# Kernel tuning notes

Hardware: AMD Instinct MI355X
Metric: run time of the kernel (lower is better)

Reference implementation:

```python
import jax, jax.numpy as jnp
import numpy as np

N_EDGES = 1_250_000
N_NODES = 100_000
EDGE_DIM = 64
N_RADIAL = 16
OUT_DIM = 1


def setup_inputs() -> dict:
    key = jax.random.key(0)
    ks = jax.random.split(key, 12)
    s_e = 1.0 / np.sqrt(EDGE_DIM)
    s_r = 1.0 / np.sqrt(N_RADIAL)
    return {
        "x": jax.random.normal(ks[0], (N_EDGES, EDGE_DIM), jnp.float32),
        "rbf": jax.random.uniform(ks[1], (N_EDGES, N_RADIAL), jnp.float32),
        "idx_i": jax.random.randint(ks[2], (N_EDGES,), 0, N_NODES, jnp.int64),
        "num_nodes": N_NODES,
        # rbf_dense: Dense(n_radial, edge_dim, bias=False) -> weight (edge_dim, n_radial)
        "W_rbf": jax.random.normal(ks[3], (EDGE_DIM, N_RADIAL), jnp.float32) * s_r,
        # three hidden Dense(edge_dim, edge_dim) with bias
        "W1": jax.random.normal(ks[4], (EDGE_DIM, EDGE_DIM), jnp.float32) * s_e,
        "b1": jnp.zeros((EDGE_DIM,), jnp.float32),
        "W2": jax.random.normal(ks[5], (EDGE_DIM, EDGE_DIM), jnp.float32) * s_e,
        "b2": jnp.zeros((EDGE_DIM,), jnp.float32),
        "W3": jax.random.normal(ks[6], (EDGE_DIM, EDGE_DIM), jnp.float32) * s_e,
        "b3": jnp.zeros((EDGE_DIM,), jnp.float32),
        # final Dense(edge_dim, out_dim, bias=False) -> weight (out_dim, edge_dim)
        "W_out": jax.random.normal(ks[7], (OUT_DIM, EDGE_DIM), jnp.float32) * s_e,
    }


def swish(h):
    # Swish(beta=1.0): h * sigmoid(h)
    return h * jax.nn.sigmoid(h)


def reference(x, rbf, idx_i, num_nodes, W_rbf, W1, b1, W2, b2, W3, b3, W_out):
    # edge gating: Dense(rbf) * x  -> (n_edge, edge_dim)
    e = (rbf @ W_rbf.T) * x
    # scatter-add edges to center nodes -> (n_node, edge_dim)
    h = jax.ops.segment_sum(e, idx_i, num_segments=num_nodes)
    h = swish(h @ W1.T + b1)
    h = swish(h @ W2.T + b2)
    h = swish(h @ W3.T + b3)
    return h @ W_out.T
```

## Files before the change

kernel.cpp:

```cpp
#include <hip/hip_runtime.h>
#include <cstdint>



__global__ __launch_bounds__(256) void k_hist(
    const int* __restrict__ idx, int* __restrict__ counts, int n_edges)
{
    const int i = blockIdx.x * blockDim.x + threadIdx.x;
    const int stride = gridDim.x * blockDim.x;
    for (int e = i; e < n_edges; e += stride)
        atomicAdd(&counts[idx[e]], 1);
}

__global__ __launch_bounds__(256) void k_scan1(
    const int* __restrict__ counts, int* __restrict__ offsets,
    int* __restrict__ blocksum, int n_nodes)
{
    __shared__ int sh[256];
    const int t = threadIdx.x;
    const int i = blockIdx.x * 256 + t;
    const int v = (i < n_nodes) ? counts[i] : 0;
    sh[t] = v;
    __syncthreads();
    for (int off = 1; off < 256; off <<= 1) {
        const int add = (t >= off) ? sh[t - off] : 0;
        __syncthreads();
        sh[t] += add;
        __syncthreads();
    }
    if (i < n_nodes) offsets[i] = sh[t] - v;
    if (t == 255) blocksum[blockIdx.x] = sh[255];
}

__global__ __launch_bounds__(512) void k_scan2(int* __restrict__ blocksum, int nb)
{
    __shared__ int sh[512];
    const int t = threadIdx.x;
    const int v = (t < nb) ? blocksum[t] : 0;
    sh[t] = v;
    __syncthreads();
    for (int off = 1; off < 512; off <<= 1) {
        const int add = (t >= off) ? sh[t - off] : 0;
        __syncthreads();
        sh[t] += add;
        __syncthreads();
    }
    if (t < nb) blocksum[t] = sh[t] - v;
}

__global__ __launch_bounds__(256) void k_addbase(
    int* __restrict__ offsets, const int* __restrict__ blocksum,
    int* __restrict__ cursor, int n_nodes, int n_edges)
{
    const int i = blockIdx.x * 256 + threadIdx.x;
    if (i < n_nodes) {
        const int o = offsets[i] + blocksum[blockIdx.x];
        offsets[i] = o;
        cursor[i]  = o;
    }
    if (i == 0) offsets[n_nodes] = n_edges;
}

__global__ __launch_bounds__(256) void k_scatter(
    const int* __restrict__ idx, int* __restrict__ cursor,
    int* __restrict__ perm, int n_edges)
{
    const int i = blockIdx.x * blockDim.x + threadIdx.x;
    const int stride = gridDim.x * blockDim.x;
    for (int e = i; e < n_edges; e += stride) {
        const int pos = atomicAdd(&cursor[idx[e]], 1);
        perm[pos] = e;
    }
}

__global__ __launch_bounds__(256) void k_gather(
    const float* __restrict__ x,
    const float* __restrict__ rbf,
    const int*   __restrict__ offsets,
    const int*   __restrict__ perm,
    const float* __restrict__ Wrbf,
    float* __restrict__ hacc,
    int n_nodes)
{
    const int lane = threadIdx.x & 63;
    const int n    = blockIdx.x * (blockDim.x >> 6) + (threadIdx.x >> 6);
    if (n >= n_nodes) return;

    float w[16];
    {
        const float4* wp = (const float4*)(Wrbf + (size_t)lane * 16);
        float4 a = wp[0], b = wp[1], c = wp[2], d = wp[3];
        w[0]=a.x; w[1]=a.y; w[2]=a.z; w[3]=a.w;
        w[4]=b.x; w[5]=b.y; w[6]=b.z; w[7]=b.w;
        w[8]=c.x; w[9]=c.y; w[10]=c.z; w[11]=c.w;
        w[12]=d.x; w[13]=d.y; w[14]=d.z; w[15]=d.w;
    }

    const int s     = offsets[n];
    const int e_end = offsets[n + 1];

    float acc = 0.0f;
    int e = (s < e_end) ? perm[s] : 0;
    for (int j = s; j < e_end; ++j) {
        const int e_nxt = (j + 1 < e_end) ? perm[j + 1] : 0;

        const float4* rp = (const float4*)(rbf + (size_t)e * 16);
        float4 r0 = rp[0], r1 = rp[1], r2 = rp[2], r3 = rp[3];
        const float xv = x[(size_t)e * 64 + lane];

        float g = 0.0f;
        g = fmaf(r0.x, w[0],  g); g = fmaf(r0.y, w[1],  g);
        g = fmaf(r0.z, w[2],  g); g = fmaf(r0.w, w[3],  g);
        g = fmaf(r1.x, w[4],  g); g = fmaf(r1.y, w[5],  g);
        g = fmaf(r1.z, w[6],  g); g = fmaf(r1.w, w[7],  g);
        g = fmaf(r2.x, w[8],  g); g = fmaf(r2.y, w[9],  g);
        g = fmaf(r2.z, w[10], g); g = fmaf(r2.w, w[11], g);
        g = fmaf(r3.x, w[12], g); g = fmaf(r3.y, w[13], g);
        g = fmaf(r3.z, w[14], g); g = fmaf(r3.w, w[15], g);

        acc = fmaf(g, xv, acc);
        e = e_nxt;
    }
    hacc[(size_t)n * 64 + lane] = acc;
}

__global__ __launch_bounds__(256) void edge_kernel(
    const float* __restrict__ x, const float* __restrict__ rbf,
    const int* __restrict__ idx, const float* __restrict__ Wrbf,
    float* __restrict__ hacc, int n_edges, int n_nodes)
{
    const int lane   = threadIdx.x & 63;
    const int wave   = blockIdx.x * (blockDim.x >> 6) + (threadIdx.x >> 6);
    const int nwaves = gridDim.x * (blockDim.x >> 6);

    float w[16];
    {
        const float4* wp = (const float4*)(Wrbf + (size_t)lane * 16);
        float4 a = wp[0], b = wp[1], c = wp[2], d = wp[3];
        w[0]=a.x; w[1]=a.y; w[2]=a.z; w[3]=a.w;
        w[4]=b.x; w[5]=b.y; w[6]=b.z; w[7]=b.w;
        w[8]=c.x; w[9]=c.y; w[10]=c.z; w[11]=c.w;
        w[12]=d.x; w[13]=d.y; w[14]=d.z; w[15]=d.w;
    }

    for (int e = wave; e < n_edges; e += nwaves) {
        const int node = idx[e];
        const float4* rp = (const float4*)(rbf + (size_t)e * 16);
        float4 r0 = rp[0], r1 = rp[1], r2 = rp[2], r3 = rp[3];
        float rv[16] = { r0.x, r0.y, r0.z, r0.w, r1.x, r1.y, r1.z, r1.w,
                         r2.x, r2.y, r2.z, r2.w, r3.x, r3.y, r3.z, r3.w };
        float g = 0.0f;
#pragma unroll
        for (int r = 0; r < 16; ++r) g = fmaf(rv[r], w[r], g);
        const float xv = x[(size_t)e * 64 + lane];
        if ((unsigned)node < (unsigned)n_nodes)
            atomicAdd(&hacc[(size_t)node * 64 + lane], g * xv);
    }
}

__device__ __forceinline__ float mlp_layer(const float* __restrict__ WT,
                                           const float* __restrict__ bias,
                                           float h, int lane)
{
    float acc = bias[lane];
#pragma unroll
    for (int k = 0; k < 64; ++k) {
        const float wk = WT[k * 64 + lane];
        const float hk = __int_as_float(
            __builtin_amdgcn_readlane(__float_as_int(h), k));
        acc = fmaf(wk, hk, acc);
    }
    return acc / (1.0f + __expf(-acc));
}

__global__ __launch_bounds__(256) void node_kernel(
    const float* __restrict__ hacc,
    const float* __restrict__ W1, const float* __restrict__ b1,
    const float* __restrict__ W2, const float* __restrict__ b2,
    const float* __restrict__ W3, const float* __restrict__ b3,
    const float* __restrict__ Wout,
    float* __restrict__ out, int n_nodes)
{
    __shared__ float WT[3][64 * 64];
    __shared__ float bs[3][64];
    __shared__ float wo[64];

    const int t = threadIdx.x;
    for (int i = t; i < 64 * 64; i += 256) {
        const int d = i & 63;
        const int k = i >> 6;
        WT[0][k * 64 + d] = W1[d * 64 + k];
        WT[1][k * 64 + d] = W2[d * 64 + k];
        WT[2][k * 64 + d] = W3[d * 64 + k];
    }
    if (t < 64) {
        bs[0][t] = b1[t]; bs[1][t] = b2[t]; bs[2][t] = b3[t];
        wo[t] = Wout[t];
    }
    __syncthreads();

    const int lane   = t & 63;
    const int wave   = blockIdx.x * (blockDim.x >> 6) + (t >> 6);
    const int nwaves = gridDim.x * (blockDim.x >> 6);

    for (int node = wave; node < n_nodes; node += nwaves) {
        float h = hacc[(size_t)node * 64 + lane];
        h = mlp_layer(WT[0], bs[0], h, lane);
        h = mlp_layer(WT[1], bs[1], h, lane);
        h = mlp_layer(WT[2], bs[2], h, lane);

        float v = wo[lane] * h;
#pragma unroll
        for (int off = 32; off >= 1; off >>= 1) v += __shfl_xor(v, off, 64);
        if (lane == 0) out[node] = v;
    }
}

extern "C" void kernel_launch(void* const* d_in, const int* in_sizes, int n_in,
                              void* d_out, int out_size, void* d_ws, size_t ws_size,
                              hipStream_t stream)
{
    const float* x    = (const float*)d_in[0];
    const float* rbf  = (const float*)d_in[1];
    const int*   idx  = (const int*)d_in[2];
    const float* Wrbf = (const float*)d_in[4];
    const float* W1   = (const float*)d_in[5];
    const float* b1   = (const float*)d_in[6];
    const float* W2   = (const float*)d_in[7];
    const float* b2   = (const float*)d_in[8];
    const float* W3   = (const float*)d_in[9];
    const float* b3   = (const float*)d_in[10];
    const float* Wout = (const float*)d_in[11];

    const int n_edges = in_sizes[0] / 64;
    const int n_nodes = out_size;

    const size_t N_pad = ((size_t)n_nodes + 1 + 63) & ~(size_t)63;
    const size_t E_pad = ((size_t)n_edges + 63) & ~(size_t)63;
    int*   counts = (int*)d_ws;
    int*   offs   = counts + N_pad;
    int*   bsum   = offs + N_pad;
    int*   perm   = bsum + 512;
    float* hacc   = (float*)(perm + E_pad);

    const size_t need = (2 * N_pad + 512 + E_pad) * sizeof(int)
                      + (size_t)n_nodes * 64 * sizeof(float);

    const int NB = (n_nodes + 255) / 256;

    if (ws_size >= need && NB <= 512) {
        hipMemsetAsync(counts, 0, (size_t)n_nodes * sizeof(int), stream);
        k_hist   <<<2048, 256, 0, stream>>>(idx, counts, n_edges);
        k_scan1  <<<NB,   256, 0, stream>>>(counts, offs, bsum, n_nodes);
        k_scan2  <<<1,    512, 0, stream>>>(bsum, NB);
        k_addbase<<<NB,   256, 0, stream>>>(offs, bsum, counts, n_nodes, n_edges);
        k_scatter<<<2048, 256, 0, stream>>>(idx, counts, perm, n_edges);

        const int gblocks = (n_nodes + 3) / 4;
        k_gather<<<gblocks, 256, 0, stream>>>(x, rbf, offs, perm, Wrbf,
                                              hacc, n_nodes);
    } else {
        hacc = (float*)d_ws;
        hipMemsetAsync(hacc, 0, (size_t)n_nodes * 64 * sizeof(float), stream);
        edge_kernel<<<8192, 256, 0, stream>>>(x, rbf, idx, Wrbf, hacc,
                                              n_edges, n_nodes);
    }

    node_kernel<<<2048, 256, 0, stream>>>(hacc, W1, b1, W2, b2, W3, b3, Wout,
                                          (float*)d_out, n_nodes);
}
```

Measured before the change: 956.7 us.

## Replace per-node wave MLP with 64-node register-tiled GEMM blocks

The node MLP used to give each wave one node and broadcast activations with readlane across 64 serial FMAs per layer. It now processes 64 nodes per block, with each thread computing a 4x4 output tile from float4 loads of activations held in shared memory (ping-pong buffers). Weights are read straight from global memory instead of being transposed into LDS, which removes the per-block 48KB transpose setup. This raises arithmetic intensity, at the cost of global or L2 weight reads and extra block syncs.

```diff
diff --git a/kernel.cpp b/kernel.cpp
--- a/kernel.cpp
+++ b/kernel.cpp
@@ -158,22 +158,42 @@
     }
 }
 
-__device__ __forceinline__ float mlp_layer(const float* __restrict__ WT,
-                                           const float* __restrict__ bias,
-                                           float h, int lane)
-{
-    float acc = bias[lane];
-#pragma unroll
-    for (int k = 0; k < 64; ++k) {
-        const float wk = WT[k * 64 + lane];
-        const float hk = __int_as_float(
-            __builtin_amdgcn_readlane(__float_as_int(h), k));
-        acc = fmaf(wk, hk, acc);
-    }
-    return acc / (1.0f + __expf(-acc));
-}
-
-__global__ __launch_bounds__(256) void node_kernel(
+__device__ __forceinline__ void gemm_tile(
+    const float (*__restrict__ Hin)[68], const float* __restrict__ Wg,
+    int n0, int d0, float acc[4][4])
+{
+#pragma unroll
+    for (int i = 0; i < 4; ++i)
+#pragma unroll
+        for (int j = 0; j < 4; ++j) acc[i][j] = 0.0f;
+
+#pragma unroll 2
+    for (int k4 = 0; k4 < 16; ++k4) {
+        float4 h4[4], w4[4];
+#pragma unroll
+        for (int i = 0; i < 4; ++i)
+            h4[i] = *(const float4*)(&Hin[n0 + i][k4 * 4]);
+#pragma unroll
+        for (int j = 0; j < 4; ++j)
+            w4[j] = *(const float4*)(Wg + (size_t)(d0 + j) * 64 + k4 * 4);
+#pragma unroll
+        for (int i = 0; i < 4; ++i)
+#pragma unroll
+            for (int j = 0; j < 4; ++j) {
+                acc[i][j] = fmaf(h4[i].x, w4[j].x, acc[i][j]);
+                acc[i][j] = fmaf(h4[i].y, w4[j].y, acc[i][j]);
+                acc[i][j] = fmaf(h4[i].z, w4[j].z, acc[i][j]);
+                acc[i][j] = fmaf(h4[i].w, w4[j].w, acc[i][j]);
+            }
+    }
+}
+
+__device__ __forceinline__ float swish_f(float v)
+{
+    return v / (1.0f + __expf(-v));
+}
+
+__global__ __launch_bounds__(256) void node_gemm(
     const float* __restrict__ hacc,
     const float* __restrict__ W1, const float* __restrict__ b1,
     const float* __restrict__ W2, const float* __restrict__ b2,
@@ -181,38 +201,93 @@
     const float* __restrict__ Wout,
     float* __restrict__ out, int n_nodes)
 {
-    __shared__ float WT[3][64 * 64];
-    __shared__ float bs[3][64];
-    __shared__ float wo[64];
-
-    const int t = threadIdx.x;
-    for (int i = t; i < 64 * 64; i += 256) {
-        const int d = i & 63;
-        const int k = i >> 6;
-        WT[0][k * 64 + d] = W1[d * 64 + k];
-        WT[1][k * 64 + d] = W2[d * 64 + k];
-        WT[2][k * 64 + d] = W3[d * 64 + k];
-    }
+    __shared__ float Ha[64][68];
+    __shared__ float Hb[64][68];
+    __shared__ float bsh[3][64];
+    __shared__ float wosh[64];
+
+    const int t    = threadIdx.x;
+    const int base = blockIdx.x * 64;
+
     if (t < 64) {
-        bs[0][t] = b1[t]; bs[1][t] = b2[t]; bs[2][t] = b3[t];
-        wo[t] = Wout[t];
-    }
-    __syncthreads();
-
-    const int lane   = t & 63;
-    const int wave   = blockIdx.x * (blockDim.x >> 6) + (t >> 6);
-    const int nwaves = gridDim.x * (blockDim.x >> 6);
-
-    for (int node = wave; node < n_nodes; node += nwaves) {
-        float h = hacc[(size_t)node * 64 + lane];
-        h = mlp_layer(WT[0], bs[0], h, lane);
-        h = mlp_layer(WT[1], bs[1], h, lane);
-        h = mlp_layer(WT[2], bs[2], h, lane);
-
-        float v = wo[lane] * h;
-#pragma unroll
-        for (int off = 32; off >= 1; off >>= 1) v += __shfl_xor(v, off, 64);
-        if (lane == 0) out[node] = v;
+        bsh[0][t] = b1[t];
+        bsh[1][t] = b2[t];
+        bsh[2][t] = b3[t];
+        wosh[t]   = Wout[t];
+    }
+
+    {
+        const int tc = t & 15;
+        const int r0 = t >> 4;
+#pragma unroll
+        for (int rr = 0; rr < 4; ++rr) {
+            const int r    = r0 + rr * 16;
+            const int node = base + r;
+            float4 v = make_float4(0.f, 0.f, 0.f, 0.f);
+            if (node < n_nodes)
+                v = *(const float4*)(hacc + (size_t)node * 64 + tc * 4);
+            *(float4*)(&Ha[r][tc * 4]) = v;
+        }
+    }
+    __syncthreads();
+
+    const int lane = t & 63;
+    const int w    = t >> 6;
+    const int td   = lane & 15;
+    const int tn   = (lane >> 4) + (w << 2);
+    const int d0   = td * 4;
+    const int n0   = tn * 4;
+
+    float acc[4][4];
+
+    gemm_tile(Ha, W1, n0, d0, acc);
+#pragma unroll
+    for (int i = 0; i < 4; ++i) {
+        float4 o;
+        o.x = swish_f(acc[i][0] + bsh[0][d0 + 0]);
+        o.y = swish_f(acc[i][1] + bsh[0][d0 + 1]);
+        o.z = swish_f(acc[i][2] + bsh[0][d0 + 2]);
+        o.w = swish_f(acc[i][3] + bsh[0][d0 + 3]);
+        *(float4*)(&Hb[n0 + i][d0]) = o;
+    }
+    __syncthreads();
+
+    gemm_tile(Hb, W2, n0, d0, acc);
+#pragma unroll
+    for (int i = 0; i < 4; ++i) {
+        float4 o;
+        o.x = swish_f(acc[i][0] + bsh[1][d0 + 0]);
+        o.y = swish_f(acc[i][1] + bsh[1][d0 + 1]);
+        o.z = swish_f(acc[i][2] + bsh[1][d0 + 2]);
+        o.w = swish_f(acc[i][3] + bsh[1][d0 + 3]);
+        *(float4*)(&Ha[n0 + i][d0]) = o;
+    }
+    __syncthreads();
+
+    gemm_tile(Ha, W3, n0, d0, acc);
+    float p[4];
+#pragma unroll
+    for (int i = 0; i < 4; ++i) {
+        float s = 0.0f;
+        s = fmaf(swish_f(acc[i][0] + bsh[2][d0 + 0]), wosh[d0 + 0], s);
+        s = fmaf(swish_f(acc[i][1] + bsh[2][d0 + 1]), wosh[d0 + 1], s);
+        s = fmaf(swish_f(acc[i][2] + bsh[2][d0 + 2]), wosh[d0 + 2], s);
+        s = fmaf(swish_f(acc[i][3] + bsh[2][d0 + 3]), wosh[d0 + 3], s);
+        p[i] = s;
+    }
+#pragma unroll
+    for (int i = 0; i < 4; ++i) {
+        p[i] += __shfl_xor(p[i], 8, 64);
+        p[i] += __shfl_xor(p[i], 4, 64);
+        p[i] += __shfl_xor(p[i], 2, 64);
+        p[i] += __shfl_xor(p[i], 1, 64);
+    }
+    if (td == 0) {
+#pragma unroll
+        for (int i = 0; i < 4; ++i) {
+            const int node = base + n0 + i;
+            if (node < n_nodes) out[node] = p[i];
+        }
     }
 }
 
@@ -266,6 +341,7 @@
                                               n_edges, n_nodes);
     }
 
-    node_kernel<<<2048, 256, 0, stream>>>(hacc, W1, b1, W2, b2, W3, b3, Wout,
-                                          (float*)d_out, n_nodes);
-}
+    const int mlp_blocks = (n_nodes + 63) / 64;
+    node_gemm<<<mlp_blocks, 256, 0, stream>>>(hacc, W1, b1, W2, b2, W3, b3,
+                                              Wout, (float*)d_out, n_nodes);
+}
```

After: 983.3 us. +2.8%, slower.
